# Optimization experiments

Measured on AMD Instinct MI355X. Metric: run time of the kernel, lower is better.

The kernel has to match this reference:

```python
import jax, jax.numpy as jnp
import numpy as np

EPS = 1e-07


def unfold(a, p):
    # torch F.unfold(a, p, padding=(p-1)//2, stride=1): [B,C,H,W] -> [B, C*p*p, H*W]
    B, C, H, W = a.shape
    pad = (p - 1) // 2
    ap = jnp.pad(a, ((0, 0), (0, 0), (pad, pad), (pad, pad)))
    # channel ordering is C-major then (kh, kw), matching torch unfold
    patches = jnp.stack([ap[:, :, i:i + H, j:j + W] for i in range(p) for j in range(p)], axis=2)
    return patches.reshape(B, C * p * p, H * W)


def linear_attn(q, k, x):
    # q:[B,h,l1,d1]  k:[B,h,l2,d1]  x:[B,h,l2,d2]
    l1, d1 = q.shape[-2:]
    l2, d2 = x.shape[-2:]
    kt = jnp.swapaxes(k, -2, -1)  # [B,h,d1,l2]
    if l1 * d1 * l2 + l1 * l2 * d2 <= d2 * l2 * d1 + d2 * d1 * l1:
        s = q @ kt                                        # [B,h,l1,l2]
        s = s / (s.sum(axis=-1, keepdims=True) + EPS)
        return s @ x
    else:
        out = q @ (kt @ x)                                # [B,h,l1,d2]
        denom = q @ kt.sum(axis=-1, keepdims=True) + EPS  # [B,h,l1,1]
        return out / denom


def setup_inputs() -> dict:
    key = jax.random.key(0)
    k1, k2, k3, k4, k5 = jax.random.split(key, 5)
    B, C, H, W = 4, 64, 128, 128
    x = jax.random.normal(k1, (B, C, H, W), dtype=jnp.float32)
    qkv_w = jax.random.normal(k2, (3 * C, C), dtype=jnp.float32) * 0.05
    qkv_b = jax.random.normal(k3, (3 * C,), dtype=jnp.float32) * 0.01
    proj_w = jax.random.normal(k4, (C, C, 3, 3), dtype=jnp.float32) * 0.05
    proj_b = jax.random.normal(k5, (C,), dtype=jnp.float32) * 0.01
    return {"x": x, "qkv_w": qkv_w, "qkv_b": qkv_b, "proj_w": proj_w, "proj_b": proj_b}


def reference(x, qkv_w, qkv_b, proj_w, proj_b):
    numHeads, patchSize = 8, 3
    B, C, H, W = x.shape
    L = H * W
    # 1x1 conv qkv
    qkv = jnp.einsum('bchw,oc->bohw', x, qkv_w) + qkv_b[None, :, None, None]
    q, k, v = qkv[:, :C], qkv[:, C:2 * C], qkv[:, 2 * C:]
    q = jax.nn.relu(q)
    k = jax.nn.relu(k)
    q = unfold(q, patchSize)  # [B, C*p*p, L]
    k = unfold(k, patchSize)
    v = v.reshape(B, C, L)
    d1 = C * patchSize * patchSize
    assert d1 % numHeads == 0  # chosen so replicate-pad branch is skipped
    q = jnp.swapaxes(q.reshape(B, numHeads, d1 // numHeads, L), -1, -2)   # [B,h,L,d1h]
    k = jnp.swapaxes(k.reshape(B, numHeads, d1 // numHeads, L), -1, -2)
    v = jnp.swapaxes(v.reshape(B, numHeads, C // numHeads, L), -1, -2)    # [B,h,L,d2h]
    out = linear_attn(q, k, v)                                            # [B,h,L,d2h]
    out = jnp.swapaxes(out, -1, -2).reshape(B, C, H, W)
    # 3x3 conv proj, padding 1
    out = jax.lax.conv_general_dilated(out, proj_w, window_strides=(1, 1), padding='SAME',
                                       dimension_numbers=('NCHW', 'OIHW', 'NCHW'))
    out = out + proj_b[None, :, None, None]
    return out
```

## Files before the change

kernel.cpp:

```cpp
#include <hip/hip_runtime.h>
#include <hip/hip_fp16.h>

#define LL 16384
#define HH 128
#define WW 128
#define CC 64
#define NH 8
#define EPSF 1e-7f
#define KVCHUNKS 32

typedef __attribute__((ext_vector_type(8))) _Float16 f16x8;
typedef __attribute__((ext_vector_type(4))) float f32x4;
typedef __attribute__((ext_vector_type(8))) unsigned short u16x8;

__global__ void qkv_kernel(const float* __restrict__ x, const float* __restrict__ w,
                           const float* __restrict__ bias,
                           float* __restrict__ q, float* __restrict__ k, float* __restrict__ v) {
    const int pix0 = blockIdx.x * 128;
    const int b    = blockIdx.y;
    const int sec  = blockIdx.z;
    const int tid  = threadIdx.x;
    const int lane = tid & 63;
    const int wv   = tid >> 6;

    __shared__ _Float16 xh[128][72], xl[128][72];
    __shared__ _Float16 wh[64][72],  wl[64][72];

    {
        const float* xb = x + (size_t)b * CC * LL + pix0;
        for (int idx = tid; idx < 64 * 128; idx += 256) {
            const int ci = idx >> 7;
            const int px = idx & 127;
            const float vv = xb[(size_t)ci * LL + px];
            const _Float16 h = (_Float16)vv;
            xh[px][ci] = h;
            xl[px][ci] = (_Float16)(vv - (float)h);
        }
    }
    {
        const float* wsec = w + (size_t)sec * 64 * 64;
        for (int idx = tid; idx < 64 * 64; idx += 256) {
            const int co = idx >> 6;
            const int ci = idx & 63;
            const float vv = wsec[co * 64 + ci];
            const _Float16 h = (_Float16)vv;
            wh[co][ci] = h;
            wl[co][ci] = (_Float16)(vv - (float)h);
        }
    }
    __syncthreads();

    f32x4 acc[4][2];
#pragma unroll
    for (int ct = 0; ct < 4; ++ct)
#pragma unroll
        for (int pt = 0; pt < 2; ++pt) acc[ct][pt] = (f32x4)0.f;

    const int g8 = (lane >> 4) * 8;
    const int rl = lane & 15;

#pragma unroll
    for (int ks = 0; ks < 2; ++ks) {
        const int kb = ks * 32 + g8;
        f16x8 ah[4], al[4], bh[2], bl[2];
#pragma unroll
        for (int ct = 0; ct < 4; ++ct) {
            ah[ct] = *(const f16x8*)&wh[ct * 16 + rl][kb];
            al[ct] = *(const f16x8*)&wl[ct * 16 + rl][kb];
        }
#pragma unroll
        for (int pt = 0; pt < 2; ++pt) {
            bh[pt] = *(const f16x8*)&xh[wv * 32 + pt * 16 + rl][kb];
            bl[pt] = *(const f16x8*)&xl[wv * 32 + pt * 16 + rl][kb];
        }
#pragma unroll
        for (int ct = 0; ct < 4; ++ct)
#pragma unroll
            for (int pt = 0; pt < 2; ++pt) {
                acc[ct][pt] = __builtin_amdgcn_mfma_f32_16x16x32_f16(ah[ct], bh[pt], acc[ct][pt], 0, 0, 0);
                acc[ct][pt] = __builtin_amdgcn_mfma_f32_16x16x32_f16(ah[ct], bl[pt], acc[ct][pt], 0, 0, 0);
                acc[ct][pt] = __builtin_amdgcn_mfma_f32_16x16x32_f16(al[ct], bh[pt], acc[ct][pt], 0, 0, 0);
            }
    }

    float* dst = (sec == 0) ? q : (sec == 1) ? k : v;
    const bool do_relu = (sec < 2);
#pragma unroll
    for (int ct = 0; ct < 4; ++ct) {
        const int co_b = ct * 16 + (lane >> 4) * 4;
#pragma unroll
        for (int pt = 0; pt < 2; ++pt) {
            const int px = pix0 + wv * 32 + pt * 16 + rl;
#pragma unroll
            for (int j = 0; j < 4; ++j) {
                const int co = co_b + j;
                float val = acc[ct][pt][j] + bias[sec * 64 + co];
                if (do_relu) val = fmaxf(val, 0.f);
                dst[((size_t)b * 64 + co) * LL + px] = val;
            }
        }
    }
}

__global__ void kv_kernel(const float* __restrict__ k, const float* __restrict__ v,
                          float* __restrict__ KVp) {
    const int chunk = blockIdx.x;
    const int h = blockIdx.y;
    const int b = blockIdx.z;
    const int tid = threadIdx.x;
    const int c  = tid >> 5;
    const int s  = tid & 31;
    const int half = s >> 4;
    const int sl   = s & 15;
    const int cpb  = half * 4;

    __shared__ float klds[8][6][130];

    {
        const float* kb = k + ((size_t)(b * 64) + 8 * h) * LL;
        for (int t = tid; t < 8 * 6 * 130; t += 256) {
            const int ch = t / 780;
            const int r1 = t - ch * 780;
            const int lr = r1 / 130;
            const int cx = r1 - lr * 130;
            const int gy = chunk * 4 + lr - 1;
            const int gx = cx - 1;
            const bool ok = (gy >= 0 && gy < HH && gx >= 0 && gx < WW);
            klds[ch][lr][cx] = ok ? kb[(size_t)ch * LL + gy * WW + gx] : 0.f;
        }
    }
    __syncthreads();

    const float* vb = v + ((size_t)(b * 64) + 8 * h + cpb) * LL;

    float kv4[9][4] = {{0.f}};
    float ks[9] = {0.f};

    for (int r = 0; r < 4; ++r) {
        const int y = chunk * 4 + r;
        for (int g = 0; g < 8; ++g) {
            const int col = g * 16 + sl;
            float vv[4];
#pragma unroll
            for (int cp = 0; cp < 4; ++cp) vv[cp] = vb[(size_t)cp * LL + y * WW + col];
            float k9[9];
#pragma unroll
            for (int dy = 0; dy < 3; ++dy)
#pragma unroll
                for (int dx = 0; dx < 3; ++dx)
                    k9[dy * 3 + dx] = klds[c][r + dy][col + dx];
#pragma unroll
            for (int p = 0; p < 9; ++p) {
                ks[p] += k9[p];
#pragma unroll
                for (int cp = 0; cp < 4; ++cp)
                    kv4[p][cp] = fmaf(k9[p], vv[cp], kv4[p][cp]);
            }
        }
    }

#pragma unroll
    for (int p = 0; p < 9; ++p) {
#pragma unroll
        for (int m = 8; m >= 1; m >>= 1) ks[p] += __shfl_xor(ks[p], m);
#pragma unroll
        for (int cp = 0; cp < 4; ++cp) {
#pragma unroll
            for (int m = 8; m >= 1; m >>= 1) kv4[p][cp] += __shfl_xor(kv4[p][cp], m);
        }
    }

    if (sl == 0) {
        float* dst = KVp + (((size_t)(b * NH + h) * KVCHUNKS) + chunk) * 648;
#pragma unroll
        for (int p = 0; p < 9; ++p) {
#pragma unroll
            for (int cp = 0; cp < 4; ++cp)
                dst[(c * 9 + p) * 8 + cpb + cp] = kv4[p][cp];
            if (half == 0) dst[576 + c * 9 + p] = ks[p];
        }
    }
}

__global__ void kv_finalize(const float* __restrict__ KVp,
                            float* __restrict__ KV, float* __restrict__ KS) {
    const int bh = blockIdx.x;
    const float* src = KVp + (size_t)bh * KVCHUNKS * 648;
    for (int idx = threadIdx.x; idx < 648; idx += 256) {
        float s0 = 0.f, s1 = 0.f, s2 = 0.f, s3 = 0.f;
#pragma unroll
        for (int ch = 0; ch < KVCHUNKS; ch += 4) {
            s0 += src[(ch + 0) * 648 + idx];
            s1 += src[(ch + 1) * 648 + idx];
            s2 += src[(ch + 2) * 648 + idx];
            s3 += src[(ch + 3) * 648 + idx];
        }
        const float sum = (s0 + s1) + (s2 + s3);
        if (idx < 576) KV[(size_t)bh * 576 + idx] = sum;
        else           KS[(size_t)bh * 72 + (idx - 576)] = sum;
    }
}

__global__ void attn_kernel(const float* __restrict__ q, const float* __restrict__ KV,
                            const float* __restrict__ KS, unsigned int* __restrict__ aohl) {
    const int y = blockIdx.x;
    const int h = blockIdx.y;
    const int b = blockIdx.z;
    const int col = threadIdx.x;

    float out[8] = {0.f};
    float den = 0.f;
    const int kvbase = (b * NH + h) * 8;

    for (int c = 0; c < 8; ++c) {
        const float* qc = q + ((size_t)(b * 64) + 8 * h + c) * LL;
        float q9[9];
#pragma unroll
        for (int dy = -1; dy <= 1; ++dy)
#pragma unroll
            for (int dx = -1; dx <= 1; ++dx) {
                const int yy = y + dy, xx = col + dx;
                const bool ok = (yy >= 0 && yy < HH && xx >= 0 && xx < WW);
                q9[(dy + 1) * 3 + (dx + 1)] = ok ? qc[yy * WW + xx] : 0.f;
            }
        const float* kvr = KV + ((size_t)(kvbase + c) * 9) * 8;
        const float* ksr = KS + (size_t)(kvbase + c) * 9;
#pragma unroll
        for (int p = 0; p < 9; ++p) {
            const float qv = q9[p];
            den += qv * ksr[p];
#pragma unroll
            for (int cp = 0; cp < 8; ++cp) out[cp] += qv * kvr[p * 8 + cp];
        }
    }
    const float inv = 1.f / (den + EPSF);
    const int pix = y * WW + col;
#pragma unroll
    for (int cp = 0; cp < 8; ++cp) {
        const float val = out[cp] * inv;
        const _Float16 hf = (_Float16)val;
        const _Float16 lf = (_Float16)(val - (float)hf);
        unsigned short hb, lb;
        __builtin_memcpy(&hb, &hf, 2);
        __builtin_memcpy(&lb, &lf, 2);
        aohl[((size_t)(b * 64) + h * 8 + cp) * LL + pix] = (unsigned int)hb | ((unsigned int)lb << 16);
    }
}

__global__ void wprep_kernel(const float* __restrict__ w, unsigned short* __restrict__ wfrag) {
    const int idx = blockIdx.x * 256 + threadIdx.x;
    const int k  = idx & 63;
    const int co = (idx >> 6) & 63;
    const int ks = idx >> 12;
    const int kg = ks * 64 + k;
    const int ci = kg >> 4, tap = kg & 15;
    const float vv = (tap < 9) ? w[(co * 64 + ci) * 9 + tap] : 0.f;
    const _Float16 h = (_Float16)vv;
    const _Float16 l = (_Float16)(vv - (float)h);
    unsigned short hb, lb;
    __builtin_memcpy(&hb, &h, 2);
    __builtin_memcpy(&lb, &l, 2);
    const int kx = (((k >> 3) ^ (co & 7)) << 3) | (k & 7);
    wfrag[(((size_t)ks * 2 + 0) * 64 + co) * 64 + kx] = hb;
    wfrag[(((size_t)ks * 2 + 1) * 64 + co) * 64 + kx] = lb;
}

__global__ __launch_bounds__(256) void conv_kernel(const unsigned int* __restrict__ aohl,
                                                   const unsigned short* __restrict__ wfrag,
                                                   const float* __restrict__ bias,
                                                   float* __restrict__ out) {
    const int bid = blockIdx.x;
    const int swz = (bid & 7) * 64 + (bid >> 3);
    const int y = swz & 127;
    const int b = swz >> 7;
    const int tid = threadIdx.x;
    const int lane = tid & 63;
    const int wv = tid >> 6;
    const int rl = lane & 15;
    const int g  = lane >> 4;

    __shared__ unsigned short plds[2 * 128 * 64];
    __shared__ unsigned short wlds[2 * 64 * 64];

    f32x4 acc[4][2];
#pragma unroll
    for (int ct = 0; ct < 4; ++ct)
#pragma unroll
        for (int pt = 0; pt < 2; ++pt) acc[ct][pt] = (f32x4)0.f;

    const unsigned int* aob = aohl + (size_t)b * 64 * LL;

    for (int ks = 0; ks < 16; ++ks) {
        __syncthreads();
        {
            const uint4* wsrc = (const uint4*)(wfrag + (size_t)ks * 8192);
            uint4* wdst = (uint4*)&wlds[0];
#pragma unroll
            for (int i = 0; i < 4; ++i) wdst[i * 256 + tid] = wsrc[i * 256 + tid];
        }
#pragma unroll
        for (int sidx = 0; sidx < 2; ++sidx) {
            const int slot = sidx * 256 + tid;
            const int pix = slot & 127;
            const int cisel = slot >> 7;
            const int ci = ks * 4 + cisel;
            const unsigned int* src = aob + (size_t)ci * LL;
            unsigned int p9[9];
#pragma unroll
            for (int dy = 0; dy < 3; ++dy) {
                const int yy = y + dy - 1;
#pragma unroll
                for (int dx = 0; dx < 3; ++dx) {
                    const int xx = pix + dx - 1;
                    const bool ok = (yy >= 0 && yy < HH && xx >= 0 && xx < WW);
                    p9[dy * 3 + dx] = ok ? src[yy * WW + xx] : 0u;
                }
            }
            unsigned short h16[16], l16[16];
#pragma unroll
            for (int j = 0; j < 16; ++j) {
                const unsigned int pv = (j < 9) ? p9[j] : 0u;
                h16[j] = (unsigned short)(pv & 0xffffu);
                l16[j] = (unsigned short)(pv >> 16);
            }
            const int x0 = (((2 * cisel)     ^ (pix & 7)) << 3);
            const int x1 = (((2 * cisel + 1) ^ (pix & 7)) << 3);
            *(u16x8*)&plds[(0 * 128 + pix) * 64 + x0] = *(u16x8*)&h16[0];
            *(u16x8*)&plds[(0 * 128 + pix) * 64 + x1] = *(u16x8*)&h16[8];
            *(u16x8*)&plds[(1 * 128 + pix) * 64 + x0] = *(u16x8*)&l16[0];
            *(u16x8*)&plds[(1 * 128 + pix) * 64 + x1] = *(u16x8*)&l16[8];
        }
        __syncthreads();

#pragma unroll
        for (int ksub = 0; ksub < 2; ++ksub) {
            const int xs = (((ksub * 4 + g) ^ (rl & 7)) << 3);
            f16x8 bh[2], bl[2];
#pragma unroll
            for (int pt = 0; pt < 2; ++pt) {
                const int row = wv * 32 + pt * 16 + rl;
                bh[pt] = *(const f16x8*)&plds[(0 * 128 + row) * 64 + xs];
                bl[pt] = *(const f16x8*)&plds[(1 * 128 + row) * 64 + xs];
            }
#pragma unroll
            for (int ct = 0; ct < 4; ++ct) {
                const int rowa = ct * 16 + rl;
                const f16x8 ah = *(const f16x8*)&wlds[(0 * 64 + rowa) * 64 + xs];
                const f16x8 al = *(const f16x8*)&wlds[(1 * 64 + rowa) * 64 + xs];
#pragma unroll
                for (int pt = 0; pt < 2; ++pt) {
                    acc[ct][pt] = __builtin_amdgcn_mfma_f32_16x16x32_f16(ah, bh[pt], acc[ct][pt], 0, 0, 0);
                    acc[ct][pt] = __builtin_amdgcn_mfma_f32_16x16x32_f16(ah, bl[pt], acc[ct][pt], 0, 0, 0);
                    acc[ct][pt] = __builtin_amdgcn_mfma_f32_16x16x32_f16(al, bh[pt], acc[ct][pt], 0, 0, 0);
                }
            }
        }
    }

#pragma unroll
    for (int ct = 0; ct < 4; ++ct) {
        const int co_b = ct * 16 + (lane >> 4) * 4;
#pragma unroll
        for (int pt = 0; pt < 2; ++pt) {
            const int px = wv * 32 + pt * 16 + rl;
#pragma unroll
            for (int j = 0; j < 4; ++j) {
                const int co = co_b + j;
                out[((size_t)b * 64 + co) * LL + y * WW + px] = acc[ct][pt][j] + bias[co];
            }
        }
    }
}

extern "C" void kernel_launch(void* const* d_in, const int* in_sizes, int n_in,
                              void* d_out, int out_size, void* d_ws, size_t ws_size,
                              hipStream_t stream) {
    const float* x      = (const float*)d_in[0];
    const float* qkv_w  = (const float*)d_in[1];
    const float* qkv_b  = (const float*)d_in[2];
    const float* proj_w = (const float*)d_in[3];
    const float* proj_b = (const float*)d_in[4];
    float* out = (float*)d_out;
    float* ws  = (float*)d_ws;

    const size_t n1 = (size_t)4 * 64 * LL;
    float* qb   = ws;
    float* kb   = ws + n1;
    float* vb   = ws + 2 * n1;
    unsigned int* aohl = (unsigned int*)(ws + 3 * n1);
    float* KV   = ws + 4 * n1;
    float* KS   = KV + 4 * 8 * 8 * 9 * 8;
    float* KVp  = KS + 4 * 8 * 8 * 9;
    unsigned short* wfrag = (unsigned short*)(KVp + (size_t)32 * KVCHUNKS * 648);

    wprep_kernel<<<256, 256, 0, stream>>>(proj_w, wfrag);
    qkv_kernel<<<dim3(128, 4, 3), 256, 0, stream>>>(x, qkv_w, qkv_b, qb, kb, vb);
    kv_kernel<<<dim3(KVCHUNKS, NH, 4), 256, 0, stream>>>(kb, vb, KVp);
    kv_finalize<<<32, 256, 0, stream>>>(KVp, KV, KS);
    attn_kernel<<<dim3(128, NH, 4), 128, 0, stream>>>(qb, KV, KS, aohl);
    conv_kernel<<<512, 256, 0, stream>>>(aohl, wfrag, proj_b, out);
}
```

Before: 117.7 us.

## Stage q halo in LDS for attention and pipeline half-row conv tiles

```diff
diff --git a/kernel.cpp b/kernel.cpp
--- a/kernel.cpp
+++ b/kernel.cpp
@@ -208,21 +208,34 @@
     const int b = blockIdx.z;
     const int col = threadIdx.x;
 
+    __shared__ float qlds[8][3][132];
+
+    {
+        const float* qbase = q + ((size_t)(b * 64) + 8 * h) * LL;
+        for (int t = threadIdx.x; t < 8 * 3 * 130; t += 128) {
+            const int c  = t / 390;
+            const int r1 = t - c * 390;
+            const int lr = r1 / 130;
+            const int cx = r1 - lr * 130;
+            const int gy = y + lr - 1;
+            const int gx = cx - 1;
+            const bool ok = (gy >= 0 && gy < HH && gx >= 0 && gx < WW);
+            qlds[c][lr][cx] = ok ? qbase[(size_t)c * LL + gy * WW + gx] : 0.f;
+        }
+    }
+    __syncthreads();
+
     float out[8] = {0.f};
     float den = 0.f;
     const int kvbase = (b * NH + h) * 8;
 
     for (int c = 0; c < 8; ++c) {
-        const float* qc = q + ((size_t)(b * 64) + 8 * h + c) * LL;
         float q9[9];
 #pragma unroll
-        for (int dy = -1; dy <= 1; ++dy)
-#pragma unroll
-            for (int dx = -1; dx <= 1; ++dx) {
-                const int yy = y + dy, xx = col + dx;
-                const bool ok = (yy >= 0 && yy < HH && xx >= 0 && xx < WW);
-                q9[(dy + 1) * 3 + (dx + 1)] = ok ? qc[yy * WW + xx] : 0.f;
-            }
+        for (int dy = 0; dy < 3; ++dy)
+#pragma unroll
+            for (int dx = 0; dx < 3; ++dx)
+                q9[dy * 3 + dx] = qlds[c][dy][col + dx];
         const float* kvr = KV + ((size_t)(kvbase + c) * 9) * 8;
         const float* ksr = KS + (size_t)(kvbase + c) * 9;
 #pragma unroll
@@ -270,52 +283,54 @@
                                                    const float* __restrict__ bias,
                                                    float* __restrict__ out) {
     const int bid = blockIdx.x;
-    const int swz = (bid & 7) * 64 + (bid >> 3);
-    const int y = swz & 127;
-    const int b = swz >> 7;
+    const int swz = (bid & 7) * 128 + (bid >> 3);
+    const int b = swz >> 8;
+    const int rem = swz & 255;
+    const int y = rem >> 1;
+    const int colbase = (rem & 1) * 64;
     const int tid = threadIdx.x;
     const int lane = tid & 63;
     const int wv = tid >> 6;
     const int rl = lane & 15;
     const int g  = lane >> 4;
 
-    __shared__ unsigned short plds[2 * 128 * 64];
+    __shared__ unsigned short plds[2 * 64 * 64];
     __shared__ unsigned short wlds[2 * 64 * 64];
 
-    f32x4 acc[4][2];
-#pragma unroll
-    for (int ct = 0; ct < 4; ++ct)
-#pragma unroll
-        for (int pt = 0; pt < 2; ++pt) acc[ct][pt] = (f32x4)0.f;
+    f32x4 acc[4];
+#pragma unroll
+    for (int ct = 0; ct < 4; ++ct) acc[ct] = (f32x4)0.f;
 
     const unsigned int* aob = aohl + (size_t)b * 64 * LL;
+    const int spix = tid & 63;
+    const int scis = tid >> 6;
+
+    unsigned int p9[9];
+    uint4 wreg[4];
+
+    auto prefetch = [&](int ks) {
+        const int ci = ks * 4 + scis;
+        const unsigned int* src = aob + (size_t)ci * LL;
+#pragma unroll
+        for (int dy = 0; dy < 3; ++dy) {
+            const int yy = y + dy - 1;
+#pragma unroll
+            for (int dx = 0; dx < 3; ++dx) {
+                const int xx = colbase + spix + dx - 1;
+                const bool ok = (yy >= 0 && yy < HH && xx >= 0 && xx < WW);
+                p9[dy * 3 + dx] = ok ? src[yy * WW + xx] : 0u;
+            }
+        }
+        const uint4* wsrc = (const uint4*)(wfrag + (size_t)ks * 8192);
+#pragma unroll
+        for (int i = 0; i < 4; ++i) wreg[i] = wsrc[i * 256 + tid];
+    };
+
+    prefetch(0);
 
     for (int ks = 0; ks < 16; ++ks) {
         __syncthreads();
         {
-            const uint4* wsrc = (const uint4*)(wfrag + (size_t)ks * 8192);
-            uint4* wdst = (uint4*)&wlds[0];
-#pragma unroll
-            for (int i = 0; i < 4; ++i) wdst[i * 256 + tid] = wsrc[i * 256 + tid];
-        }
-#pragma unroll
-        for (int sidx = 0; sidx < 2; ++sidx) {
-            const int slot = sidx * 256 + tid;
-            const int pix = slot & 127;
-            const int cisel = slot >> 7;
-            const int ci = ks * 4 + cisel;
-            const unsigned int* src = aob + (size_t)ci * LL;
-            unsigned int p9[9];
-#pragma unroll
-            for (int dy = 0; dy < 3; ++dy) {
-                const int yy = y + dy - 1;
-#pragma unroll
-                for (int dx = 0; dx < 3; ++dx) {
-                    const int xx = pix + dx - 1;
-                    const bool ok = (yy >= 0 && yy < HH && xx >= 0 && xx < WW);
-                    p9[dy * 3 + dx] = ok ? src[yy * WW + xx] : 0u;
-                }
-            }
             unsigned short h16[16], l16[16];
 #pragma unroll
             for (int j = 0; j < 16; ++j) {
@@ -323,51 +338,45 @@
                 h16[j] = (unsigned short)(pv & 0xffffu);
                 l16[j] = (unsigned short)(pv >> 16);
             }
-            const int x0 = (((2 * cisel)     ^ (pix & 7)) << 3);
-            const int x1 = (((2 * cisel + 1) ^ (pix & 7)) << 3);
-            *(u16x8*)&plds[(0 * 128 + pix) * 64 + x0] = *(u16x8*)&h16[0];
-            *(u16x8*)&plds[(0 * 128 + pix) * 64 + x1] = *(u16x8*)&h16[8];
-            *(u16x8*)&plds[(1 * 128 + pix) * 64 + x0] = *(u16x8*)&l16[0];
-            *(u16x8*)&plds[(1 * 128 + pix) * 64 + x1] = *(u16x8*)&l16[8];
+            const int x0 = (((2 * scis)     ^ (spix & 7)) << 3);
+            const int x1 = (((2 * scis + 1) ^ (spix & 7)) << 3);
+            *(u16x8*)&plds[(0 * 64 + spix) * 64 + x0] = *(u16x8*)&h16[0];
+            *(u16x8*)&plds[(0 * 64 + spix) * 64 + x1] = *(u16x8*)&h16[8];
+            *(u16x8*)&plds[(1 * 64 + spix) * 64 + x0] = *(u16x8*)&l16[0];
+            *(u16x8*)&plds[(1 * 64 + spix) * 64 + x1] = *(u16x8*)&l16[8];
+            uint4* wdst = (uint4*)&wlds[0];
+#pragma unroll
+            for (int i = 0; i < 4; ++i) wdst[i * 256 + tid] = wreg[i];
         }
         __syncthreads();
+        if (ks < 15) prefetch(ks + 1);
 
 #pragma unroll
         for (int ksub = 0; ksub < 2; ++ksub) {
             const int xs = (((ksub * 4 + g) ^ (rl & 7)) << 3);
-            f16x8 bh[2], bl[2];
-#pragma unroll
-            for (int pt = 0; pt < 2; ++pt) {
-                const int row = wv * 32 + pt * 16 + rl;
-                bh[pt] = *(const f16x8*)&plds[(0 * 128 + row) * 64 + xs];
-                bl[pt] = *(const f16x8*)&plds[(1 * 128 + row) * 64 + xs];
-            }
+            const int row = wv * 16 + rl;
+            const f16x8 bh = *(const f16x8*)&plds[(0 * 64 + row) * 64 + xs];
+            const f16x8 bl = *(const f16x8*)&plds[(1 * 64 + row) * 64 + xs];
 #pragma unroll
             for (int ct = 0; ct < 4; ++ct) {
                 const int rowa = ct * 16 + rl;
                 const f16x8 ah = *(const f16x8*)&wlds[(0 * 64 + rowa) * 64 + xs];
                 const f16x8 al = *(const f16x8*)&wlds[(1 * 64 + rowa) * 64 + xs];
-#pragma unroll
-                for (int pt = 0; pt < 2; ++pt) {
-                    acc[ct][pt] = __builtin_amdgcn_mfma_f32_16x16x32_f16(ah, bh[pt], acc[ct][pt], 0, 0, 0);
-                    acc[ct][pt] = __builtin_amdgcn_mfma_f32_16x16x32_f16(ah, bl[pt], acc[ct][pt], 0, 0, 0);
-                    acc[ct][pt] = __builtin_amdgcn_mfma_f32_16x16x32_f16(al, bh[pt], acc[ct][pt], 0, 0, 0);
-                }
+                acc[ct] = __builtin_amdgcn_mfma_f32_16x16x32_f16(ah, bh, acc[ct], 0, 0, 0);
+                acc[ct] = __builtin_amdgcn_mfma_f32_16x16x32_f16(ah, bl, acc[ct], 0, 0, 0);
+                acc[ct] = __builtin_amdgcn_mfma_f32_16x16x32_f16(al, bh, acc[ct], 0, 0, 0);
             }
         }
     }
 
 #pragma unroll
     for (int ct = 0; ct < 4; ++ct) {
-        const int co_b = ct * 16 + (lane >> 4) * 4;
-#pragma unroll
-        for (int pt = 0; pt < 2; ++pt) {
-            const int px = wv * 32 + pt * 16 + rl;
-#pragma unroll
-            for (int j = 0; j < 4; ++j) {
-                const int co = co_b + j;
-                out[((size_t)b * 64 + co) * LL + y * WW + px] = acc[ct][pt][j] + bias[co];
-            }
+        const int co_b = ct * 16 + g * 4;
+        const int px = colbase + wv * 16 + rl;
+#pragma unroll
+        for (int j = 0; j < 4; ++j) {
+            const int co = co_b + j;
+            out[((size_t)b * 64 + co) * LL + y * WW + px] = acc[ct][j] + bias[co];
         }
     }
 }
@@ -398,5 +407,5 @@
     kv_kernel<<<dim3(KVCHUNKS, NH, 4), 256, 0, stream>>>(kb, vb, KVp);
     kv_finalize<<<32, 256, 0, stream>>>(KVp, KV, KS);
     attn_kernel<<<dim3(128, NH, 4), 128, 0, stream>>>(qb, KV, KS, aohl);
-    conv_kernel<<<512, 256, 0, stream>>>(aohl, wfrag, proj_b, out);
-}
+    conv_kernel<<<1024, 256, 0, stream>>>(aohl, wfrag, proj_b, out);
+}
```

New measurement: 170.8 us. 1.45x slower.
